# Kernel tuning notes

Hardware: AMD Instinct MI355X
Metric: run time of the kernel (lower is better)

The kernel has to match this reference:

```python
import jax, jax.numpy as jnp
import numpy as np

R, K, C, T = 4096, 16384, 512, 1000

def setup_inputs() -> dict:
    key = jax.random.key(0)
    k1, k2, k3, k4 = jax.random.split(key, 4)
    x = jax.random.normal(k1, (R, 1, C), dtype=jnp.float32)
    t = jax.random.randint(k2, (R,), 0, T)
    A = jax.random.normal(k3, (K, C), dtype=jnp.float32)
    # bar_alpha in (0,1): cumulative alpha-bar diffusion schedule
    bar_alpha = jax.random.uniform(k4, (T,), dtype=jnp.float32, minval=1e-4, maxval=1.0 - 1e-4)
    return {"x": x, "t": t, "A": A, "bar_alpha": bar_alpha}

def reference(x, t, A, bar_alpha):
    # x: [R,1,C], t: [R] int, A: [K,C] codebook, bar_alpha: [T]
    xs = x[:, 0, :]                       # [R,C]
    ba = bar_alpha[t]                     # [R]
    sa = jnp.sqrt(ba)                     # sqrt(bar_alpha[t_r])
    # ||sa_r*A_k - x_r||^2 = sa^2*||A_k||^2 - 2*sa*(x_r . A_k) + ||x_r||^2
    A_sq = jnp.sum(A * A, axis=1)         # [K]
    x_sq = jnp.sum(xs * xs, axis=1)       # [R]
    xA = jnp.einsum('rc,kc->rk', xs, A)   # [R,K]
    d2 = sa[:, None] ** 2 * A_sq[None, :] - 2.0 * sa[:, None] * xA + x_sq[:, None]
    logits = -d2 / (2.0 * (1.0 - ba))[:, None]   # [R,K]
    w = jax.nn.softmax(logits, axis=1)           # per-row softmax weights
    res = jnp.einsum('rk,kc->rc', w, A)          # [R,C]
    return res[:, None, :]                        # [R,1,C]
```

## Files before the change

kernel.cpp:

```cpp
#include <hip/hip_runtime.h>
#include <cstdint>
#include <cstddef>

#define R_DIM 4096
#define K_DIM 16384
#define C_DIM 512
#define SPLITS 4
#define BM 64
#define BK 128
#define KRANGE (K_DIM / SPLITS)
#define NTILES (KRANGE / BK)
#define GTILES (K_DIM / BK)

typedef unsigned short us8 __attribute__((ext_vector_type(8)));
typedef float f32x4 __attribute__((ext_vector_type(4)));
typedef __bf16 bfv8 __attribute__((ext_vector_type(8)));

#define MFMA16(a, b, c) __builtin_amdgcn_mfma_f32_16x16x32_bf16((a), (b), (c), 0, 0, 0)
#define BC(v) __builtin_bit_cast(bfv8, (v))

__device__ __forceinline__ unsigned short f2bf(float v) {
    union { float f; unsigned u; } x; x.f = v;
    unsigned r = x.u + 0x7fffu + ((x.u >> 16) & 1u);
    return (unsigned short)(r >> 16);
}
__device__ __forceinline__ float bf2f(unsigned short b) {
    union { unsigned u; float f; } x; x.u = ((unsigned)b) << 16;
    return x.f;
}

__device__ __forceinline__ void gload16(const char* g, char* l) {
    __builtin_amdgcn_global_load_lds(
        (const __attribute__((address_space(1))) void*)g,
        (__attribute__((address_space(3))) void*)l, 16, 0, 0);
}

#define PHASE_BAR(N) do {                                                   \
    asm volatile("s_waitcnt vmcnt(" #N ") lgkmcnt(0)" ::: "memory");        \
    __builtin_amdgcn_s_barrier();                                           \
    __builtin_amdgcn_sched_barrier(0);                                      \
} while (0)

#define OFF_IMGA ((size_t)0)
#define OFF_IMGC ((size_t)33554432)
#define OFF_XH   ((size_t)67108864)
#define OFF_XL   ((size_t)71303168)
#define OFF_ASQ  ((size_t)75497472)
#define OFF_ROWP ((size_t)75563008)
#define OFF_PO   ((size_t)75628544)
#define OFF_PM   ((size_t)109182976)
#define OFF_PL   ((size_t)109248512)
#define WS_NEED  ((size_t)109314048)

#define SM_BUF0 0
#define SM_BUF1 32768
#define SM_BUF2 65536
#define SM_U    98304
#define SM_U2   114688
#define SM_MX   131072
#define SM_SM   131584
#define SM_TOT  132096


__global__ void k_rows(const int* __restrict__ t, const float* __restrict__ bar_alpha,
                       float4* __restrict__ rowp) {
    int r = blockIdx.x * 256 + threadIdx.x;
    if (r >= R_DIM) return;
    float ba = bar_alpha[t[r]];
    float sa = sqrtf(ba);
    float inv = 1.0f / (1.0f - ba);
    rowp[r] = make_float4(sa, 0.5f * sa * sa, inv * 1.4426950408889634f, inv);
}

__global__ void k_splitx(const float* __restrict__ x, us8* __restrict__ xh, us8* __restrict__ xl) {
    int i = blockIdx.x * 256 + threadIdx.x;
    if (i >= R_DIM * C_DIM / 8) return;
    const float4* x4 = (const float4*)x + (size_t)i * 2;
    float v[8];
    float4 a = x4[0], b = x4[1];
    v[0]=a.x; v[1]=a.y; v[2]=a.z; v[3]=a.w; v[4]=b.x; v[5]=b.y; v[6]=b.z; v[7]=b.w;
    us8 h, l;
#pragma unroll
    for (int j = 0; j < 8; ++j) {
        unsigned short hb = f2bf(v[j]);
        h[j] = hb;
        l[j] = f2bf(v[j] - bf2f(hb));
    }
    xh[i] = h; xl[i] = l;
}

__global__ __launch_bounds__(256) void k_imgA(const float* __restrict__ A, char* __restrict__ img) {
    int gt = blockIdx.x >> 3, j = blockIdx.x & 7;
    char* base = img + (size_t)blockIdx.x * 32768;
    int t = threadIdx.x;
#pragma unroll
    for (int it = 0; it < 4; ++it) {
        int p = t + it * 256;
        int kl = p >> 3, cb = p & 7;
        const float* src = A + (size_t)(gt * 128 + kl) * C_DIM + j * 64 + cb * 8;
        us8 h, l;
#pragma unroll
        for (int q = 0; q < 8; ++q) {
            float v = src[q];
            unsigned short hb = f2bf(v);
            h[q] = hb; l[q] = f2bf(v - bf2f(hb));
        }
        int pos = kl * 128 + ((cb * 16) ^ ((kl & 7) << 4));
        *(us8*)(base + pos) = h;
        *(us8*)(base + 16384 + pos) = l;
    }
}

__global__ __launch_bounds__(256) void k_imgC(const float* __restrict__ A, char* __restrict__ img) {
    int gt = blockIdx.x >> 3, j = blockIdx.x & 7;
    char* base = img + (size_t)blockIdx.x * 32768;
    int t = threadIdx.x;
#pragma unroll
    for (int it = 0; it < 4; ++it) {
        int p = t + it * 256;
        int cl = p & 63, kb = p >> 6;
        us8 h, l;
#pragma unroll
        for (int q = 0; q < 8; ++q) {
            float v = A[(size_t)(gt * 128 + kb * 8 + q) * C_DIM + j * 64 + cl];
            unsigned short hb = f2bf(v);
            h[q] = hb; l[q] = f2bf(v - bf2f(hb));
        }
        int pos = cl * 256 + ((kb * 16) ^ ((cl & 7) << 4));
        *(us8*)(base + pos) = h;
        *(us8*)(base + 16384 + pos) = l;
    }
}

__global__ void k_asq(const float* __restrict__ A, float* __restrict__ Asq) {
    int wid = threadIdx.x >> 6, lane = threadIdx.x & 63;
    int k = blockIdx.x * 4 + wid;
    const float4* a4 = (const float4*)(A + (size_t)k * C_DIM);
    float s = 0.f;
#pragma unroll
    for (int j = 0; j < 2; ++j) {
        float4 v = a4[lane * 2 + j];
        s += v.x * v.x + v.y * v.y + v.z * v.z + v.w * v.w;
    }
#pragma unroll
    for (int off = 32; off; off >>= 1) s += __shfl_xor(s, off);
    if (lane == 0) Asq[k] = s;
}

__global__ __launch_bounds__(512, 2) void k_fused(
    const char* __restrict__ imgA, const char* __restrict__ imgC,
    const unsigned short* __restrict__ xh, const unsigned short* __restrict__ xl,
    const float* __restrict__ Asq, const float4* __restrict__ rowp,
    float* __restrict__ pO, float* __restrict__ pM, float* __restrict__ pL)
{
    extern __shared__ char smem[];
    const int tid = threadIdx.x;
    const int lane = tid & 63, wid = tid >> 6;
    const int wr = wid >> 1, wc = wid & 1;
    const int l15 = lane & 15, l4 = lane >> 4;
    const int rb = (blockIdx.x >> 2) * BM;
    const int split = blockIdx.x & (SPLITS - 1);

    float sa[4], hb[4], ce[4];
#pragma unroll
    for (int q = 0; q < 4; ++q) {
        float4 p = rowp[rb + wr * 16 + l4 * 4 + q];
        sa[q] = p.x; hb[q] = p.y; ce[q] = p.z;
    }
    float Mr[4], Lr[4];
#pragma unroll
    for (int q = 0; q < 4; ++q) { Mr[q] = -1e30f; Lr[q] = 0.f; }
    f32x4 of[8][2];
#pragma unroll
    for (int a = 0; a < 8; ++a)
#pragma unroll
        for (int b = 0; b < 2; ++b) of[a][b] = (f32x4){0.f, 0.f, 0.f, 0.f};

    const int xrow = (rb + wr * 16 + l15) * C_DIM;
    const int stg = tid * 16;

    {
        const char* s0 = imgA + (size_t)(split * NTILES) * 8 * 32768;
        const char* s1 = s0 + 32768;
#pragma unroll
        for (int i = 0; i < 4; ++i) gload16(s0 + stg + i * 8192, smem + SM_BUF0 + stg + i * 8192);
#pragma unroll
        for (int i = 0; i < 4; ++i) gload16(s1 + stg + i * 8192, smem + SM_BUF1 + stg + i * 8192);
    }
    __syncthreads();
    int cur = 0;

    for (int kt = 0; kt < NTILES; ++kt) {
        const int gt = split * NTILES + kt;
        const int gtn = (kt == NTILES - 1) ? split * NTILES : gt + 1;
        const int kbase = gt * BK;
        f32x4 sf[4];
#pragma unroll
        for (int f = 0; f < 4; ++f) sf[f] = (f32x4){0.f, 0.f, 0.f, 0.f};

        us8 xbh[2][2], xbl[2][2];
#pragma unroll
        for (int j = 0; j < 8; ++j) {
            if (j == 0) {
#pragma unroll
                for (int cs = 0; cs < 2; ++cs) {
                    int off = xrow + 0 * 64 + cs * 32 + l4 * 8;
                    xbh[0][cs] = *(const us8*)(xh + off);
                    xbl[0][cs] = *(const us8*)(xl + off);
                }
            }
            if (j < 7) {
#pragma unroll
                for (int cs = 0; cs < 2; ++cs) {
                    int off = xrow + (j + 1) * 64 + cs * 32 + l4 * 8;
                    xbh[(j + 1) & 1][cs] = *(const us8*)(xh + off);
                    xbl[(j + 1) & 1][cs] = *(const us8*)(xl + off);
                }
            }
            {
                char* d = smem + ((cur + 2) % 3) * 32768 + stg;
                if (j < 6) {
                    const char* s = imgA + ((size_t)gt * 8 + j + 2) * 32768;
#pragma unroll
                    for (int i = 0; i < 4; ++i) gload16(s + stg + i * 8192, d + i * 8192);
                } else if (j == 6) {
                    const char* s = imgC + ((size_t)gt * 8 + 0) * 32768;
#pragma unroll
                    for (int i = 0; i < 2; ++i) gload16(s + stg + i * 8192, d + i * 8192);
                } else {
                    const char* s = imgC + ((size_t)gt * 8 + 1) * 32768;
#pragma unroll
                    for (int i = 0; i < 2; ++i) gload16(s + stg + i * 8192, d + i * 8192);
                }
            }
            const char* B = smem + cur * 32768;
#pragma unroll
            for (int cs = 0; cs < 2; ++cs) {
#pragma unroll
                for (int f = 0; f < 4; ++f) {
                    int row = wc * 64 + f * 16 + l15;
                    int byte = row * 128 + ((cs * 64 + l4 * 16) ^ ((row & 7) << 4));
                    bfv8 qh = *(const bfv8*)(B + byte);
                    bfv8 ql = *(const bfv8*)(B + 16384 + byte);
                    sf[f] = MFMA16(BC(xbh[j & 1][cs]), qh, sf[f]);
                    sf[f] = MFMA16(BC(xbh[j & 1][cs]), ql, sf[f]);
                    sf[f] = MFMA16(BC(xbl[j & 1][cs]), qh, sf[f]);
                }
            }
            if (j == 0)      PHASE_BAR(8);
            else if (j < 6)  PHASE_BAR(6);
            else if (j == 6) PHASE_BAR(4);
            else             PHASE_BAR(2);
            cur = (cur + 1) % 3;
        }

        float g[4][4];
#pragma unroll
        for (int f = 0; f < 4; ++f) {
            float asq = Asq[kbase + wc * 64 + f * 16 + l15];
#pragma unroll
            for (int q = 0; q < 4; ++q) g[f][q] = sa[q] * sf[f][q] - hb[q] * asq;
        }
        float tmax[4];
#pragma unroll
        for (int q = 0; q < 4; ++q)
            tmax[q] = fmaxf(fmaxf(g[0][q], g[1][q]), fmaxf(g[2][q], g[3][q]));
#pragma unroll
        for (int off = 1; off < 16; off <<= 1)
#pragma unroll
            for (int q = 0; q < 4; ++q) tmax[q] = fmaxf(tmax[q], __shfl_xor(tmax[q], off));
        float* smax = (float*)(smem + SM_MX);
        if (l15 == 0) {
#pragma unroll
            for (int q = 0; q < 4; ++q) smax[wc * 64 + wr * 16 + l4 * 4 + q] = tmax[q];
        }
        __syncthreads();
        float Mn[4], al[4];
#pragma unroll
        for (int q = 0; q < 4; ++q) {
            float other = smax[(wc ^ 1) * 64 + wr * 16 + l4 * 4 + q];
            float tm = fmaxf(tmax[q], other);
            Mn[q] = fmaxf(Mr[q], tm);
            al[q] = exp2f((Mr[q] - Mn[q]) * ce[q]);
        }
        float u[4][4], tsum[4] = {0.f, 0.f, 0.f, 0.f};
#pragma unroll
        for (int f = 0; f < 4; ++f)
#pragma unroll
            for (int q = 0; q < 4; ++q) {
                u[f][q] = exp2f((g[f][q] - Mn[q]) * ce[q]);
                tsum[q] += u[f][q];
            }
#pragma unroll
        for (int off = 1; off < 16; off <<= 1)
#pragma unroll
            for (int q = 0; q < 4; ++q) tsum[q] += __shfl_xor(tsum[q], off);
        float* ssum = (float*)(smem + SM_SM);
        if (l15 == 0) {
#pragma unroll
            for (int q = 0; q < 4; ++q) ssum[wc * 64 + wr * 16 + l4 * 4 + q] = tsum[q];
        }
#pragma unroll
        for (int f = 0; f < 4; ++f)
#pragma unroll
            for (int q = 0; q < 4; ++q) {
                int m_loc = wr * 16 + l4 * 4 + q;
                int k_loc = wc * 64 + f * 16 + l15;
                int byte = (m_loc * 256 + k_loc * 2) ^ ((m_loc & 7) << 4);
                unsigned short uh = f2bf(u[f][q]);
                *(unsigned short*)(smem + SM_U + byte) = uh;
                *(unsigned short*)(smem + SM_U2 + byte) = f2bf(u[f][q] - bf2f(uh));
            }
        __syncthreads();
#pragma unroll
        for (int q = 0; q < 4; ++q) {
            float others = ssum[(wc ^ 1) * 64 + wr * 16 + l4 * 4 + q];
            Lr[q] = Lr[q] * al[q] + tsum[q] + others;
            Mr[q] = Mn[q];
        }
#pragma unroll
        for (int a = 0; a < 8; ++a)
#pragma unroll
            for (int b = 0; b < 2; ++b)
#pragma unroll
                for (int q = 0; q < 4; ++q) of[a][b][q] *= al[q];

        us8 uhf[4], ulf[4];
#pragma unroll
        for (int ks = 0; ks < 4; ++ks) {
            int m_loc = wr * 16 + l15;
            int byte = (m_loc * 256 + ks * 64 + l4 * 16) ^ ((m_loc & 7) << 4);
            uhf[ks] = *(const us8*)(smem + SM_U + byte);
            ulf[ks] = *(const us8*)(smem + SM_U2 + byte);
        }
#pragma unroll
        for (int j = 0; j < 8; ++j) {
            {
                char* d = smem + ((cur + 2) % 3) * 32768 + stg;
                if (j < 6) {
                    const char* s = imgC + ((size_t)gt * 8 + j + 2) * 32768;
#pragma unroll
                    for (int i = 0; i < 2; ++i) gload16(s + stg + i * 8192, d + i * 8192);
                } else {
                    const char* s = imgA + ((size_t)gtn * 8 + (j - 6)) * 32768;
#pragma unroll
                    for (int i = 0; i < 4; ++i) gload16(s + stg + i * 8192, d + i * 8192);
                }
            }
            const char* B = smem + cur * 32768;
#pragma unroll
            for (int f = 0; f < 2; ++f) {
                int cl = wc * 32 + f * 16 + l15;
#pragma unroll
                for (int ks = 0; ks < 4; ++ks) {
                    int byte = cl * 256 + ((ks * 64 + l4 * 16) ^ ((cl & 7) << 4));
                    bfv8 qh = *(const bfv8*)(B + byte);
                    of[j][f] = MFMA16(BC(uhf[ks]), qh, of[j][f]);
                    of[j][f] = MFMA16(BC(ulf[ks]), qh, of[j][f]);
                }
            }
            if (j < 6) PHASE_BAR(2);
            else       PHASE_BAR(4);
            cur = (cur + 1) % 3;
        }
    }

#pragma unroll
    for (int j = 0; j < 8; ++j)
#pragma unroll
        for (int f = 0; f < 2; ++f)
#pragma unroll
            for (int q = 0; q < 4; ++q) {
                int gm = rb + wr * 16 + l4 * 4 + q;
                int cg = j * 64 + wc * 32 + f * 16 + l15;
                pO[((size_t)gm * SPLITS + split) * C_DIM + cg] = of[j][f][q];
            }
    if (wc == 0 && l15 == 0) {
#pragma unroll
        for (int q = 0; q < 4; ++q) {
            int gm = rb + wr * 16 + l4 * 4 + q;
            pM[gm * SPLITS + split] = Mr[q];
            pL[gm * SPLITS + split] = Lr[q];
        }
    }
}

__global__ void k_combine(const float* __restrict__ pO, const float* __restrict__ pM,
                          const float* __restrict__ pL, const float4* __restrict__ rowp,
                          float* __restrict__ out) {
    int r = blockIdx.x;
    int tid = threadIdx.x;
    float ce = rowp[r].z;
    float Ms[SPLITS], Ls[SPLITS];
    float M = -1e30f;
#pragma unroll
    for (int s = 0; s < SPLITS; ++s) {
        Ms[s] = pM[r * SPLITS + s];
        Ls[s] = pL[r * SPLITS + s];
        M = fmaxf(M, Ms[s]);
    }
    float es[SPLITS], L = 0.f;
#pragma unroll
    for (int s = 0; s < SPLITS; ++s) { es[s] = exp2f((Ms[s] - M) * ce); L += Ls[s] * es[s]; }
    float invL = 1.0f / L;
    f32x4 acc = (f32x4){0.f, 0.f, 0.f, 0.f};
#pragma unroll
    for (int s = 0; s < SPLITS; ++s) {
        f32x4 v = *(const f32x4*)(pO + ((size_t)r * SPLITS + s) * C_DIM + tid * 4);
        acc += v * es[s];
    }
    acc *= invL;
    *(f32x4*)(out + (size_t)r * C_DIM + tid * 4) = acc;
}

extern "C" void kernel_launch(void* const* d_in, const int* in_sizes, int n_in,
                              void* d_out, int out_size, void* d_ws, size_t ws_size,
                              hipStream_t stream) {
    const float* x = (const float*)d_in[0];
    const int* t = (const int*)d_in[1];
    const float* A = (const float*)d_in[2];
    const float* bar_alpha = (const float*)d_in[3];
    float* out = (float*)d_out;
    char* ws = (char*)d_ws;
    if (ws_size < WS_NEED) return;

    char* imgA = ws + OFF_IMGA;
    char* imgC = ws + OFF_IMGC;
    unsigned short* Xh = (unsigned short*)(ws + OFF_XH);
    unsigned short* Xl = (unsigned short*)(ws + OFF_XL);
    float* Asq = (float*)(ws + OFF_ASQ);
    float4* rowp = (float4*)(ws + OFF_ROWP);
    float* pO = (float*)(ws + OFF_PO);
    float* pM = (float*)(ws + OFF_PM);
    float* pL = (float*)(ws + OFF_PL);

    (void)hipFuncSetAttribute((const void*)k_fused,
                              hipFuncAttributeMaxDynamicSharedMemorySize, SM_TOT);

    k_rows<<<R_DIM / 256, 256, 0, stream>>>(t, bar_alpha, rowp);
    k_splitx<<<(R_DIM * C_DIM / 8) / 256, 256, 0, stream>>>(x, (us8*)Xh, (us8*)Xl);
    k_imgA<<<GTILES * 8, 256, 0, stream>>>(A, imgA);
    k_imgC<<<GTILES * 8, 256, 0, stream>>>(A, imgC);
    k_asq<<<K_DIM / 4, 256, 0, stream>>>(A, Asq);
    k_fused<<<(R_DIM / BM) * SPLITS, 512, SM_TOT, stream>>>(imgA, imgC, Xh, Xl,
                                                            Asq, rowp, pO, pM, pL);
    k_combine<<<R_DIM, 128, 0, stream>>>(pO, pM, pL, rowp, out);
}
```

Before: 537.2 us.

## Switch fused softmax-attention kernel to 32x32x16 MFMA with 2x4 wave tiling

Rewrites the fused kernel to use 32x32x16 bf16 MFMA tiles instead of 16x16x32, remapping the eight waves from 4x2 to 2x4 (rows x keys). The per-wave fragment layout, the softmax max/sum reductions (now across four key-waves through shared memory), the P-matrix swizzled store, and the second GEMM's C-tile staging (two C chunks per phase, four phases) all change to match. The goal is fewer MFMA instructions and fewer LDS operand reads per FLOP. The cost is more registers per wave, wider 32-lane shuffle reductions, and a uniform phase barrier count.

```diff
diff --git a/kernel.cpp b/kernel.cpp
--- a/kernel.cpp
+++ b/kernel.cpp
@@ -14,9 +14,10 @@
 
 typedef unsigned short us8 __attribute__((ext_vector_type(8)));
 typedef float f32x4 __attribute__((ext_vector_type(4)));
+typedef float f32x16 __attribute__((ext_vector_type(16)));
 typedef __bf16 bfv8 __attribute__((ext_vector_type(8)));
 
-#define MFMA16(a, b, c) __builtin_amdgcn_mfma_f32_16x16x32_bf16((a), (b), (c), 0, 0, 0)
+#define MFMA32(a, b, c) __builtin_amdgcn_mfma_f32_32x32x16_bf16((a), (b), (c), 0, 0, 0)
 #define BC(v) __builtin_bit_cast(bfv8, (v))
 
 __device__ __forceinline__ unsigned short f2bf(float v) {
@@ -58,8 +59,9 @@
 #define SM_U    98304
 #define SM_U2   114688
 #define SM_MX   131072
-#define SM_SM   131584
-#define SM_TOT  132096
+#define SM_SM   132096
+#define SM_ROWL 133120
+#define SM_TOT  133632
 
 
 __global__ void k_rows(const int* __restrict__ t, const float* __restrict__ bar_alpha,
@@ -156,27 +158,30 @@
     extern __shared__ char smem[];
     const int tid = threadIdx.x;
     const int lane = tid & 63, wid = tid >> 6;
-    const int wr = wid >> 1, wc = wid & 1;
-    const int l15 = lane & 15, l4 = lane >> 4;
+    const int wm = wid >> 2, wk = wid & 3;
+    const int l31 = lane & 31, hl = lane >> 5;
     const int rb = (blockIdx.x >> 2) * BM;
     const int split = blockIdx.x & (SPLITS - 1);
 
-    float sa[4], hb[4], ce[4];
-#pragma unroll
-    for (int q = 0; q < 4; ++q) {
-        float4 p = rowp[rb + wr * 16 + l4 * 4 + q];
-        sa[q] = p.x; hb[q] = p.y; ce[q] = p.z;
-    }
-    float Mr[4], Lr[4];
-#pragma unroll
-    for (int q = 0; q < 4; ++q) { Mr[q] = -1e30f; Lr[q] = 0.f; }
-    f32x4 of[8][2];
-#pragma unroll
-    for (int a = 0; a < 8; ++a)
-#pragma unroll
-        for (int b = 0; b < 2; ++b) of[a][b] = (f32x4){0.f, 0.f, 0.f, 0.f};
-
-    const int xrow = (rb + wr * 16 + l15) * C_DIM;
+    float2* rowl = (float2*)(smem + SM_ROWL);
+    float* smax = (float*)(smem + SM_MX);
+    float* ssum = (float*)(smem + SM_SM);
+
+    if (tid < 64) {
+        float4 p = rowp[rb + tid];
+        rowl[tid] = make_float2(p.x, p.z);
+    }
+
+    float Mr[16], Lr[16];
+#pragma unroll
+    for (int r = 0; r < 16; ++r) { Mr[r] = -1e30f; Lr[r] = 0.f; }
+    f32x16 of[4];
+#pragma unroll
+    for (int p = 0; p < 4; ++p)
+#pragma unroll
+        for (int r = 0; r < 16; ++r) of[p][r] = 0.f;
+
+    const int xrowbase = (rb + wm * 32 + l31) * C_DIM;
     const int stg = tid * 16;
 
     {
@@ -194,193 +199,173 @@
         const int gt = split * NTILES + kt;
         const int gtn = (kt == NTILES - 1) ? split * NTILES : gt + 1;
         const int kbase = gt * BK;
-        f32x4 sf[4];
-#pragma unroll
-        for (int f = 0; f < 4; ++f) sf[f] = (f32x4){0.f, 0.f, 0.f, 0.f};
-
-        us8 xbh[2][2], xbl[2][2];
+
+        f32x16 sf;
+#pragma unroll
+        for (int r = 0; r < 16; ++r) sf[r] = 0.f;
+
 #pragma unroll
         for (int j = 0; j < 8; ++j) {
-            if (j == 0) {
-#pragma unroll
-                for (int cs = 0; cs < 2; ++cs) {
-                    int off = xrow + 0 * 64 + cs * 32 + l4 * 8;
-                    xbh[0][cs] = *(const us8*)(xh + off);
-                    xbl[0][cs] = *(const us8*)(xl + off);
-                }
-            }
-            if (j < 7) {
-#pragma unroll
-                for (int cs = 0; cs < 2; ++cs) {
-                    int off = xrow + (j + 1) * 64 + cs * 32 + l4 * 8;
-                    xbh[(j + 1) & 1][cs] = *(const us8*)(xh + off);
-                    xbl[(j + 1) & 1][cs] = *(const us8*)(xl + off);
-                }
-            }
+            us8 xh8[4], xl8[4];
+#pragma unroll
+            for (int s = 0; s < 4; ++s) {
+                int xoff = xrowbase + j * 64 + s * 16 + hl * 8;
+                xh8[s] = *(const us8*)(xh + xoff);
+                xl8[s] = *(const us8*)(xl + xoff);
+            }
+            __builtin_amdgcn_sched_barrier(0);
             {
-                char* d = smem + ((cur + 2) % 3) * 32768 + stg;
+                char* d = smem + ((cur + 2) % 3) * 32768;
                 if (j < 6) {
                     const char* s = imgA + ((size_t)gt * 8 + j + 2) * 32768;
 #pragma unroll
-                    for (int i = 0; i < 4; ++i) gload16(s + stg + i * 8192, d + i * 8192);
-                } else if (j == 6) {
-                    const char* s = imgC + ((size_t)gt * 8 + 0) * 32768;
-#pragma unroll
-                    for (int i = 0; i < 2; ++i) gload16(s + stg + i * 8192, d + i * 8192);
+                    for (int i = 0; i < 4; ++i) gload16(s + stg + i * 8192, d + stg + i * 8192);
                 } else {
-                    const char* s = imgC + ((size_t)gt * 8 + 1) * 32768;
-#pragma unroll
-                    for (int i = 0; i < 2; ++i) gload16(s + stg + i * 8192, d + i * 8192);
+                    int c0 = (j - 6) * 2;
+                    const char* s0 = imgC + ((size_t)gt * 8 + c0) * 32768;
+                    const char* s1 = imgC + ((size_t)gt * 8 + c0 + 1) * 32768;
+                    gload16(s0 + stg, d + stg);
+                    gload16(s0 + stg + 8192, d + stg + 8192);
+                    gload16(s1 + stg, d + 16384 + stg);
+                    gload16(s1 + stg + 8192, d + 16384 + stg + 8192);
                 }
             }
+            __builtin_amdgcn_sched_barrier(0);
             const char* B = smem + cur * 32768;
-#pragma unroll
-            for (int cs = 0; cs < 2; ++cs) {
-#pragma unroll
-                for (int f = 0; f < 4; ++f) {
-                    int row = wc * 64 + f * 16 + l15;
-                    int byte = row * 128 + ((cs * 64 + l4 * 16) ^ ((row & 7) << 4));
-                    bfv8 qh = *(const bfv8*)(B + byte);
-                    bfv8 ql = *(const bfv8*)(B + 16384 + byte);
-                    sf[f] = MFMA16(BC(xbh[j & 1][cs]), qh, sf[f]);
-                    sf[f] = MFMA16(BC(xbh[j & 1][cs]), ql, sf[f]);
-                    sf[f] = MFMA16(BC(xbl[j & 1][cs]), qh, sf[f]);
+            const int kl = wk * 32 + l31;
+#pragma unroll
+            for (int s = 0; s < 4; ++s) {
+                int cb = 2 * s + hl;
+                int byte = kl * 128 + ((cb ^ (kl & 7)) << 4);
+                bfv8 qh = *(const bfv8*)(B + byte);
+                bfv8 ql = *(const bfv8*)(B + 16384 + byte);
+                sf = MFMA32(BC(xh8[s]), qh, sf);
+                sf = MFMA32(BC(xh8[s]), ql, sf);
+                sf = MFMA32(BC(xl8[s]), qh, sf);
+            }
+            PHASE_BAR(4);
+            cur = (cur + 1) % 3;
+        }
+
+        {
+            const int k = wk * 32 + l31;
+            const float asq = Asq[kbase + k];
+            const int kb = k >> 3;
+            float g[16], mx[16];
+#pragma unroll
+            for (int r = 0; r < 16; ++r) {
+                int ml = wm * 32 + (r & 3) + 8 * (r >> 2) + 4 * hl;
+                float sa = rowl[ml].x;
+                g[r] = sa * (sf[r] - 0.5f * sa * asq);
+                mx[r] = g[r];
+            }
+#pragma unroll
+            for (int off = 1; off < 32; off <<= 1)
+#pragma unroll
+                for (int r = 0; r < 16; ++r) mx[r] = fmaxf(mx[r], __shfl_xor(mx[r], off));
+            if (l31 == 0) {
+#pragma unroll
+                for (int r = 0; r < 16; ++r)
+                    smax[wk * 64 + wm * 32 + (r & 3) + 8 * (r >> 2) + 4 * hl] = mx[r];
+            }
+            __syncthreads();
+            float Mn[16], al[16], ts[16];
+#pragma unroll
+            for (int r = 0; r < 16; ++r) {
+                int ml = wm * 32 + (r & 3) + 8 * (r >> 2) + 4 * hl;
+                float m4 = fmaxf(fmaxf(smax[ml], smax[64 + ml]),
+                                 fmaxf(smax[128 + ml], smax[192 + ml]));
+                Mn[r] = fmaxf(Mr[r], m4);
+                float ce = rowl[ml].y;
+                al[r] = exp2f((Mr[r] - Mn[r]) * ce);
+                float u = exp2f((g[r] - Mn[r]) * ce);
+                ts[r] = u;
+                unsigned short uh = f2bf(u);
+                unsigned short ul = f2bf(u - bf2f(uh));
+                int byte = ml * 256 + ((kb ^ (ml & 7)) << 4) + (k & 7) * 2;
+                *(unsigned short*)(smem + SM_U + byte) = uh;
+                *(unsigned short*)(smem + SM_U2 + byte) = ul;
+            }
+#pragma unroll
+            for (int off = 1; off < 32; off <<= 1)
+#pragma unroll
+                for (int r = 0; r < 16; ++r) ts[r] += __shfl_xor(ts[r], off);
+            if (l31 == 0) {
+#pragma unroll
+                for (int r = 0; r < 16; ++r)
+                    ssum[wk * 64 + wm * 32 + (r & 3) + 8 * (r >> 2) + 4 * hl] = ts[r];
+            }
+            __syncthreads();
+#pragma unroll
+            for (int r = 0; r < 16; ++r) {
+                int ml = wm * 32 + (r & 3) + 8 * (r >> 2) + 4 * hl;
+                float s4 = (ssum[ml] + ssum[64 + ml]) + (ssum[128 + ml] + ssum[192 + ml]);
+                Lr[r] = Lr[r] * al[r] + s4;
+                Mr[r] = Mn[r];
+            }
+#pragma unroll
+            for (int p = 0; p < 4; ++p)
+#pragma unroll
+                for (int r = 0; r < 16; ++r) of[p][r] *= al[r];
+        }
+        bfv8 uH[8], uL[8];
+        {
+            const int m2 = wm * 32 + l31;
+#pragma unroll
+            for (int ks = 0; ks < 8; ++ks) {
+                int kb2 = ks * 2 + hl;
+                int byte = m2 * 256 + ((kb2 ^ (m2 & 7)) << 4);
+                uH[ks] = *(const bfv8*)(smem + SM_U + byte);
+                uL[ks] = *(const bfv8*)(smem + SM_U2 + byte);
+            }
+        }
+
+#pragma unroll
+        for (int p = 0; p < 4; ++p) {
+            {
+                char* d = smem + ((cur + 2) % 3) * 32768;
+                if (p < 2) {
+                    const char* s0 = imgC + ((size_t)gt * 8 + (p + 2) * 2) * 32768;
+                    const char* s1 = imgC + ((size_t)gt * 8 + (p + 2) * 2 + 1) * 32768;
+                    gload16(s0 + stg, d + stg);
+                    gload16(s0 + stg + 8192, d + stg + 8192);
+                    gload16(s1 + stg, d + 16384 + stg);
+                    gload16(s1 + stg + 8192, d + 16384 + stg + 8192);
+                } else {
+                    const char* s = imgA + ((size_t)gtn * 8 + (p - 2)) * 32768;
+#pragma unroll
+                    for (int i = 0; i < 4; ++i) gload16(s + stg + i * 8192, d + stg + i * 8192);
                 }
             }
-            if (j == 0)      PHASE_BAR(8);
-            else if (j < 6)  PHASE_BAR(6);
-            else if (j == 6) PHASE_BAR(4);
-            else             PHASE_BAR(2);
+            const char* B = smem + cur * 32768 + (wk >> 1) * 16384;
+            const int cl = (wk & 1) * 32 + l31;
+#pragma unroll
+            for (int ks = 0; ks < 8; ++ks) {
+                int kb = ks * 2 + hl;
+                int byte = cl * 256 + ((kb ^ (cl & 7)) << 4);
+                bfv8 qh = *(const bfv8*)(B + byte);
+                of[p] = MFMA32(uH[ks], qh, of[p]);
+                of[p] = MFMA32(uL[ks], qh, of[p]);
+            }
+            PHASE_BAR(4);
             cur = (cur + 1) % 3;
         }
-
-        float g[4][4];
-#pragma unroll
-        for (int f = 0; f < 4; ++f) {
-            float asq = Asq[kbase + wc * 64 + f * 16 + l15];
-#pragma unroll
-            for (int q = 0; q < 4; ++q) g[f][q] = sa[q] * sf[f][q] - hb[q] * asq;
-        }
-        float tmax[4];
-#pragma unroll
-        for (int q = 0; q < 4; ++q)
-            tmax[q] = fmaxf(fmaxf(g[0][q], g[1][q]), fmaxf(g[2][q], g[3][q]));
-#pragma unroll
-        for (int off = 1; off < 16; off <<= 1)
-#pragma unroll
-            for (int q = 0; q < 4; ++q) tmax[q] = fmaxf(tmax[q], __shfl_xor(tmax[q], off));
-        float* smax = (float*)(smem + SM_MX);
-        if (l15 == 0) {
-#pragma unroll
-            for (int q = 0; q < 4; ++q) smax[wc * 64 + wr * 16 + l4 * 4 + q] = tmax[q];
-        }
-        __syncthreads();
-        float Mn[4], al[4];
-#pragma unroll
-        for (int q = 0; q < 4; ++q) {
-            float other = smax[(wc ^ 1) * 64 + wr * 16 + l4 * 4 + q];
-            float tm = fmaxf(tmax[q], other);
-            Mn[q] = fmaxf(Mr[q], tm);
-            al[q] = exp2f((Mr[q] - Mn[q]) * ce[q]);
-        }
-        float u[4][4], tsum[4] = {0.f, 0.f, 0.f, 0.f};
-#pragma unroll
-        for (int f = 0; f < 4; ++f)
-#pragma unroll
-            for (int q = 0; q < 4; ++q) {
-                u[f][q] = exp2f((g[f][q] - Mn[q]) * ce[q]);
-                tsum[q] += u[f][q];
-            }
-#pragma unroll
-        for (int off = 1; off < 16; off <<= 1)
-#pragma unroll
-            for (int q = 0; q < 4; ++q) tsum[q] += __shfl_xor(tsum[q], off);
-        float* ssum = (float*)(smem + SM_SM);
-        if (l15 == 0) {
-#pragma unroll
-            for (int q = 0; q < 4; ++q) ssum[wc * 64 + wr * 16 + l4 * 4 + q] = tsum[q];
-        }
-#pragma unroll
-        for (int f = 0; f < 4; ++f)
-#pragma unroll
-            for (int q = 0; q < 4; ++q) {
-                int m_loc = wr * 16 + l4 * 4 + q;
-                int k_loc = wc * 64 + f * 16 + l15;
-                int byte = (m_loc * 256 + k_loc * 2) ^ ((m_loc & 7) << 4);
-                unsigned short uh = f2bf(u[f][q]);
-                *(unsigned short*)(smem + SM_U + byte) = uh;
-                *(unsigned short*)(smem + SM_U2 + byte) = f2bf(u[f][q] - bf2f(uh));
-            }
-        __syncthreads();
-#pragma unroll
-        for (int q = 0; q < 4; ++q) {
-            float others = ssum[(wc ^ 1) * 64 + wr * 16 + l4 * 4 + q];
-            Lr[q] = Lr[q] * al[q] + tsum[q] + others;
-            Mr[q] = Mn[q];
-        }
-#pragma unroll
-        for (int a = 0; a < 8; ++a)
-#pragma unroll
-            for (int b = 0; b < 2; ++b)
-#pragma unroll
-                for (int q = 0; q < 4; ++q) of[a][b][q] *= al[q];
-
-        us8 uhf[4], ulf[4];
-#pragma unroll
-        for (int ks = 0; ks < 4; ++ks) {
-            int m_loc = wr * 16 + l15;
-            int byte = (m_loc * 256 + ks * 64 + l4 * 16) ^ ((m_loc & 7) << 4);
-            uhf[ks] = *(const us8*)(smem + SM_U + byte);
-            ulf[ks] = *(const us8*)(smem + SM_U2 + byte);
-        }
-#pragma unroll
-        for (int j = 0; j < 8; ++j) {
-            {
-                char* d = smem + ((cur + 2) % 3) * 32768 + stg;
-                if (j < 6) {
-                    const char* s = imgC + ((size_t)gt * 8 + j + 2) * 32768;
-#pragma unroll
-                    for (int i = 0; i < 2; ++i) gload16(s + stg + i * 8192, d + i * 8192);
-                } else {
-                    const char* s = imgA + ((size_t)gtn * 8 + (j - 6)) * 32768;
-#pragma unroll
-                    for (int i = 0; i < 4; ++i) gload16(s + stg + i * 8192, d + i * 8192);
-                }
-            }
-            const char* B = smem + cur * 32768;
-#pragma unroll
-            for (int f = 0; f < 2; ++f) {
-                int cl = wc * 32 + f * 16 + l15;
-#pragma unroll
-                for (int ks = 0; ks < 4; ++ks) {
-                    int byte = cl * 256 + ((ks * 64 + l4 * 16) ^ ((cl & 7) << 4));
-                    bfv8 qh = *(const bfv8*)(B + byte);
-                    of[j][f] = MFMA16(BC(uhf[ks]), qh, of[j][f]);
-                    of[j][f] = MFMA16(BC(ulf[ks]), qh, of[j][f]);
-                }
-            }
-            if (j < 6) PHASE_BAR(2);
-            else       PHASE_BAR(4);
-            cur = (cur + 1) % 3;
-        }
-    }
-
-#pragma unroll
-    for (int j = 0; j < 8; ++j)
-#pragma unroll
-        for (int f = 0; f < 2; ++f)
-#pragma unroll
-            for (int q = 0; q < 4; ++q) {
-                int gm = rb + wr * 16 + l4 * 4 + q;
-                int cg = j * 64 + wc * 32 + f * 16 + l15;
-                pO[((size_t)gm * SPLITS + split) * C_DIM + cg] = of[j][f][q];
-            }
-    if (wc == 0 && l15 == 0) {
-#pragma unroll
-        for (int q = 0; q < 4; ++q) {
-            int gm = rb + wr * 16 + l4 * 4 + q;
-            pM[gm * SPLITS + split] = Mr[q];
-            pL[gm * SPLITS + split] = Lr[q];
+    }
+
+#pragma unroll
+    for (int p = 0; p < 4; ++p)
+#pragma unroll
+        for (int r = 0; r < 16; ++r) {
+            int gm = rb + wm * 32 + (r & 3) + 8 * (r >> 2) + 4 * hl;
+            int cg = p * 128 + wk * 32 + l31;
+            pO[((size_t)gm * SPLITS + split) * C_DIM + cg] = of[p][r];
+        }
+    if (wk == 0 && l31 == 0) {
+#pragma unroll
+        for (int r = 0; r < 16; ++r) {
+            int gm = rb + wm * 32 + (r & 3) + 8 * (r >> 2) + 4 * hl;
+            pM[gm * SPLITS + split] = Mr[r];
+            pL[gm * SPLITS + split] = Lr[r];
         }
     }
 }
```

Measured after the change: 1.172 ms. 118% more time.

## Split QK phase across warps along C with 2 M-fragments and smem reduction

Applied to the files above, without the earlier changes.

Changes the score-GEMM warp layout so each warp covers 32 rows (two M fragments) and half of each C chunk, reusing every loaded A fragment for two MFMA groups and halving LDS B reads per MFMA. Partial scores from the two C-halves are reduced through a staging buffer in shared memory, and only half the warps do the softmax; rescale factors are shared via a new smem array. The x split kernel writes x in a permuted layout to match the new per-warp column slicing. This adds an extra barrier and smem round trip and leaves half the warps idle during softmax.

```diff
diff --git a/kernel.cpp b/kernel.cpp
--- a/kernel.cpp
+++ b/kernel.cpp
@@ -59,7 +59,8 @@
 #define SM_U2   114688
 #define SM_MX   131072
 #define SM_SM   131584
-#define SM_TOT  132096
+#define SM_AL   132096
+#define SM_TOT  132352
 
 
 __global__ void k_rows(const int* __restrict__ t, const float* __restrict__ bar_alpha,
@@ -75,18 +76,22 @@
 __global__ void k_splitx(const float* __restrict__ x, us8* __restrict__ xh, us8* __restrict__ xl) {
     int i = blockIdx.x * 256 + threadIdx.x;
     if (i >= R_DIM * C_DIM / 8) return;
+    int r = i >> 6;
+    int c = (i & 63) * 8;
+    int ct = (c >> 5) & 1, j = c >> 6, cp = c & 31;
+    int og = (r * 512 + ct * 256 + j * 32 + cp) >> 3;
     const float4* x4 = (const float4*)x + (size_t)i * 2;
     float v[8];
     float4 a = x4[0], b = x4[1];
     v[0]=a.x; v[1]=a.y; v[2]=a.z; v[3]=a.w; v[4]=b.x; v[5]=b.y; v[6]=b.z; v[7]=b.w;
     us8 h, l;
 #pragma unroll
-    for (int j = 0; j < 8; ++j) {
-        unsigned short hb = f2bf(v[j]);
-        h[j] = hb;
-        l[j] = f2bf(v[j] - bf2f(hb));
-    }
-    xh[i] = h; xl[i] = l;
+    for (int q = 0; q < 8; ++q) {
+        unsigned short hb = f2bf(v[q]);
+        h[q] = hb;
+        l[q] = f2bf(v[q] - bf2f(hb));
+    }
+    xh[og] = h; xl[og] = l;
 }
 
 __global__ __launch_bounds__(256) void k_imgA(const float* __restrict__ A, char* __restrict__ img) {
@@ -156,27 +161,32 @@
     extern __shared__ char smem[];
     const int tid = threadIdx.x;
     const int lane = tid & 63, wid = tid >> 6;
-    const int wr = wid >> 1, wc = wid & 1;
+    const int wr2 = wid >> 2, wc = (wid >> 1) & 1, ct = wid & 1;
+    const int wrC = wid >> 1, wcC = wid & 1;
     const int l15 = lane & 15, l4 = lane >> 4;
     const int rb = (blockIdx.x >> 2) * BM;
     const int split = blockIdx.x & (SPLITS - 1);
 
-    float sa[4], hb[4], ce[4];
-#pragma unroll
-    for (int q = 0; q < 4; ++q) {
-        float4 p = rowp[rb + wr * 16 + l4 * 4 + q];
-        sa[q] = p.x; hb[q] = p.y; ce[q] = p.z;
-    }
-    float Mr[4], Lr[4];
-#pragma unroll
-    for (int q = 0; q < 4; ++q) { Mr[q] = -1e30f; Lr[q] = 0.f; }
+    float sa[2][4], hb[2][4], ce[2][4];
+#pragma unroll
+    for (int mf = 0; mf < 2; ++mf)
+#pragma unroll
+        for (int q = 0; q < 4; ++q) {
+            float4 p = rowp[rb + wr2 * 32 + mf * 16 + l4 * 4 + q];
+            sa[mf][q] = p.x; hb[mf][q] = p.y; ce[mf][q] = p.z;
+        }
+    float Mr[2][4], Lr[2][4];
+#pragma unroll
+    for (int mf = 0; mf < 2; ++mf)
+#pragma unroll
+        for (int q = 0; q < 4; ++q) { Mr[mf][q] = -1e30f; Lr[mf][q] = 0.f; }
     f32x4 of[8][2];
 #pragma unroll
     for (int a = 0; a < 8; ++a)
 #pragma unroll
         for (int b = 0; b < 2; ++b) of[a][b] = (f32x4){0.f, 0.f, 0.f, 0.f};
 
-    const int xrow = (rb + wr * 16 + l15) * C_DIM;
+    const int xb0 = (rb + wr2 * 32 + l15) * 512 + ct * 256 + l4 * 8;
     const int stg = tid * 16;
 
     {
@@ -194,29 +204,21 @@
         const int gt = split * NTILES + kt;
         const int gtn = (kt == NTILES - 1) ? split * NTILES : gt + 1;
         const int kbase = gt * BK;
-        f32x4 sf[4];
-#pragma unroll
-        for (int f = 0; f < 4; ++f) sf[f] = (f32x4){0.f, 0.f, 0.f, 0.f};
+        f32x4 sf[2][4];
+#pragma unroll
+        for (int mf = 0; mf < 2; ++mf)
+#pragma unroll
+            for (int f = 0; f < 4; ++f) sf[mf][f] = (f32x4){0.f, 0.f, 0.f, 0.f};
 
         us8 xbh[2][2], xbl[2][2];
 #pragma unroll
+        for (int mf = 0; mf < 2; ++mf) {
+            int off = xb0 + mf * 8192;
+            xbh[0][mf] = *(const us8*)(xh + off);
+            xbl[0][mf] = *(const us8*)(xl + off);
+        }
+#pragma unroll
         for (int j = 0; j < 8; ++j) {
-            if (j == 0) {
-#pragma unroll
-                for (int cs = 0; cs < 2; ++cs) {
-                    int off = xrow + 0 * 64 + cs * 32 + l4 * 8;
-                    xbh[0][cs] = *(const us8*)(xh + off);
-                    xbl[0][cs] = *(const us8*)(xl + off);
-                }
-            }
-            if (j < 7) {
-#pragma unroll
-                for (int cs = 0; cs < 2; ++cs) {
-                    int off = xrow + (j + 1) * 64 + cs * 32 + l4 * 8;
-                    xbh[(j + 1) & 1][cs] = *(const us8*)(xh + off);
-                    xbl[(j + 1) & 1][cs] = *(const us8*)(xl + off);
-                }
-            }
             {
                 char* d = smem + ((cur + 2) % 3) * 32768 + stg;
                 if (j < 6) {
@@ -233,18 +235,26 @@
                     for (int i = 0; i < 2; ++i) gload16(s + stg + i * 8192, d + i * 8192);
                 }
             }
+            if (j < 7) {
+#pragma unroll
+                for (int mf = 0; mf < 2; ++mf) {
+                    int off = xb0 + mf * 8192 + (j + 1) * 32;
+                    xbh[(j + 1) & 1][mf] = *(const us8*)(xh + off);
+                    xbl[(j + 1) & 1][mf] = *(const us8*)(xl + off);
+                }
+            }
             const char* B = smem + cur * 32768;
 #pragma unroll
-            for (int cs = 0; cs < 2; ++cs) {
-#pragma unroll
-                for (int f = 0; f < 4; ++f) {
-                    int row = wc * 64 + f * 16 + l15;
-                    int byte = row * 128 + ((cs * 64 + l4 * 16) ^ ((row & 7) << 4));
-                    bfv8 qh = *(const bfv8*)(B + byte);
-                    bfv8 ql = *(const bfv8*)(B + 16384 + byte);
-                    sf[f] = MFMA16(BC(xbh[j & 1][cs]), qh, sf[f]);
-                    sf[f] = MFMA16(BC(xbh[j & 1][cs]), ql, sf[f]);
-                    sf[f] = MFMA16(BC(xbl[j & 1][cs]), qh, sf[f]);
+            for (int f = 0; f < 4; ++f) {
+                int row = wc * 64 + f * 16 + l15;
+                int byte = row * 128 + ((ct * 64 + l4 * 16) ^ ((row & 7) << 4));
+                bfv8 qh = *(const bfv8*)(B + byte);
+                bfv8 ql = *(const bfv8*)(B + 16384 + byte);
+#pragma unroll
+                for (int mf = 0; mf < 2; ++mf) {
+                    sf[mf][f] = MFMA16(BC(xbh[j & 1][mf]), qh, sf[mf][f]);
+                    sf[mf][f] = MFMA16(BC(xbh[j & 1][mf]), ql, sf[mf][f]);
+                    sf[mf][f] = MFMA16(BC(xbl[j & 1][mf]), qh, sf[mf][f]);
                 }
             }
             if (j == 0)      PHASE_BAR(8);
@@ -254,85 +264,130 @@
             cur = (cur + 1) % 3;
         }
 
-        float g[4][4];
-#pragma unroll
-        for (int f = 0; f < 4; ++f) {
-            float asq = Asq[kbase + wc * 64 + f * 16 + l15];
-#pragma unroll
-            for (int q = 0; q < 4; ++q) g[f][q] = sa[q] * sf[f][q] - hb[q] * asq;
-        }
-        float tmax[4];
-#pragma unroll
-        for (int q = 0; q < 4; ++q)
-            tmax[q] = fmaxf(fmaxf(g[0][q], g[1][q]), fmaxf(g[2][q], g[3][q]));
-#pragma unroll
-        for (int off = 1; off < 16; off <<= 1)
-#pragma unroll
-            for (int q = 0; q < 4; ++q) tmax[q] = fmaxf(tmax[q], __shfl_xor(tmax[q], off));
+        float* mrg = (float*)(smem + ((cur + 2) % 3) * 32768);
+        const int mslot = ((wr2 * 2 + wc) * 64 + lane) * 4;
+        if (ct == 1) {
+#pragma unroll
+            for (int mf = 0; mf < 2; ++mf)
+#pragma unroll
+                for (int f = 0; f < 4; ++f)
+                    *(f32x4*)(mrg + (mf * 4 + f) * 1024 + mslot) = sf[mf][f];
+        }
+        __syncthreads();
+
         float* smax = (float*)(smem + SM_MX);
-        if (l15 == 0) {
-#pragma unroll
-            for (int q = 0; q < 4; ++q) smax[wc * 64 + wr * 16 + l4 * 4 + q] = tmax[q];
+        float* ssum = (float*)(smem + SM_SM);
+        float* alL = (float*)(smem + SM_AL);
+        float g[2][4][4], Mn[2][4], al[2][4], ts[2][4];
+        if (ct == 0) {
+            float asq[4];
+#pragma unroll
+            for (int f = 0; f < 4; ++f) asq[f] = Asq[kbase + wc * 64 + f * 16 + l15];
+            float tmax[2][4];
+#pragma unroll
+            for (int mf = 0; mf < 2; ++mf)
+#pragma unroll
+                for (int f = 0; f < 4; ++f) {
+                    sf[mf][f] += *(const f32x4*)(mrg + (mf * 4 + f) * 1024 + mslot);
+#pragma unroll
+                    for (int q = 0; q < 4; ++q)
+                        g[mf][f][q] = sa[mf][q] * sf[mf][f][q] - hb[mf][q] * asq[f];
+                }
+#pragma unroll
+            for (int mf = 0; mf < 2; ++mf)
+#pragma unroll
+                for (int q = 0; q < 4; ++q)
+                    tmax[mf][q] = fmaxf(fmaxf(g[mf][0][q], g[mf][1][q]),
+                                        fmaxf(g[mf][2][q], g[mf][3][q]));
+#pragma unroll
+            for (int off = 1; off < 16; off <<= 1)
+#pragma unroll
+                for (int mf = 0; mf < 2; ++mf)
+#pragma unroll
+                    for (int q = 0; q < 4; ++q)
+                        tmax[mf][q] = fmaxf(tmax[mf][q], __shfl_xor(tmax[mf][q], off));
+            if (l15 == 0) {
+#pragma unroll
+                for (int mf = 0; mf < 2; ++mf)
+#pragma unroll
+                    for (int q = 0; q < 4; ++q)
+                        smax[wc * 64 + wr2 * 32 + mf * 16 + l4 * 4 + q] = tmax[mf][q];
+            }
         }
         __syncthreads();
-        float Mn[4], al[4];
-#pragma unroll
-        for (int q = 0; q < 4; ++q) {
-            float other = smax[(wc ^ 1) * 64 + wr * 16 + l4 * 4 + q];
-            float tm = fmaxf(tmax[q], other);
-            Mn[q] = fmaxf(Mr[q], tm);
-            al[q] = exp2f((Mr[q] - Mn[q]) * ce[q]);
-        }
-        float u[4][4], tsum[4] = {0.f, 0.f, 0.f, 0.f};
-#pragma unroll
-        for (int f = 0; f < 4; ++f)
-#pragma unroll
-            for (int q = 0; q < 4; ++q) {
-                u[f][q] = exp2f((g[f][q] - Mn[q]) * ce[q]);
-                tsum[q] += u[f][q];
-            }
-#pragma unroll
-        for (int off = 1; off < 16; off <<= 1)
-#pragma unroll
-            for (int q = 0; q < 4; ++q) tsum[q] += __shfl_xor(tsum[q], off);
-        float* ssum = (float*)(smem + SM_SM);
-        if (l15 == 0) {
-#pragma unroll
-            for (int q = 0; q < 4; ++q) ssum[wc * 64 + wr * 16 + l4 * 4 + q] = tsum[q];
-        }
-#pragma unroll
-        for (int f = 0; f < 4; ++f)
-#pragma unroll
-            for (int q = 0; q < 4; ++q) {
-                int m_loc = wr * 16 + l4 * 4 + q;
-                int k_loc = wc * 64 + f * 16 + l15;
-                int byte = (m_loc * 256 + k_loc * 2) ^ ((m_loc & 7) << 4);
-                unsigned short uh = f2bf(u[f][q]);
-                *(unsigned short*)(smem + SM_U + byte) = uh;
-                *(unsigned short*)(smem + SM_U2 + byte) = f2bf(u[f][q] - bf2f(uh));
-            }
+        if (ct == 0) {
+#pragma unroll
+            for (int mf = 0; mf < 2; ++mf)
+#pragma unroll
+                for (int q = 0; q < 4; ++q) {
+                    int row = wr2 * 32 + mf * 16 + l4 * 4 + q;
+                    float tm = fmaxf(smax[row], smax[64 + row]);
+                    Mn[mf][q] = fmaxf(Mr[mf][q], tm);
+                    al[mf][q] = exp2f((Mr[mf][q] - Mn[mf][q]) * ce[mf][q]);
+                    ts[mf][q] = 0.f;
+                }
+#pragma unroll
+            for (int mf = 0; mf < 2; ++mf)
+#pragma unroll
+                for (int f = 0; f < 4; ++f)
+#pragma unroll
+                    for (int q = 0; q < 4; ++q) {
+                        float u = exp2f((g[mf][f][q] - Mn[mf][q]) * ce[mf][q]);
+                        ts[mf][q] += u;
+                        int m_loc = wr2 * 32 + mf * 16 + l4 * 4 + q;
+                        int k_loc = wc * 64 + f * 16 + l15;
+                        int byte = (m_loc * 256 + k_loc * 2) ^ ((m_loc & 7) << 4);
+                        unsigned short uh = f2bf(u);
+                        *(unsigned short*)(smem + SM_U + byte) = uh;
+                        *(unsigned short*)(smem + SM_U2 + byte) = f2bf(u - bf2f(uh));
+                    }
+#pragma unroll
+            for (int off = 1; off < 16; off <<= 1)
+#pragma unroll
+                for (int mf = 0; mf < 2; ++mf)
+#pragma unroll
+                    for (int q = 0; q < 4; ++q) ts[mf][q] += __shfl_xor(ts[mf][q], off);
+            if (l15 == 0) {
+#pragma unroll
+                for (int mf = 0; mf < 2; ++mf)
+#pragma unroll
+                    for (int q = 0; q < 4; ++q) {
+                        int row = wr2 * 32 + mf * 16 + l4 * 4 + q;
+                        ssum[wc * 64 + row] = ts[mf][q];
+                        if (wc == 0) alL[row] = al[mf][q];
+                    }
+            }
+        }
         __syncthreads();
-#pragma unroll
-        for (int q = 0; q < 4; ++q) {
-            float others = ssum[(wc ^ 1) * 64 + wr * 16 + l4 * 4 + q];
-            Lr[q] = Lr[q] * al[q] + tsum[q] + others;
-            Mr[q] = Mn[q];
-        }
+        if (ct == 0) {
+#pragma unroll
+            for (int mf = 0; mf < 2; ++mf)
+#pragma unroll
+                for (int q = 0; q < 4; ++q) {
+                    int row = wr2 * 32 + mf * 16 + l4 * 4 + q;
+                    float others = ssum[(wc ^ 1) * 64 + row];
+                    Lr[mf][q] = Lr[mf][q] * al[mf][q] + ts[mf][q] + others;
+                    Mr[mf][q] = Mn[mf][q];
+                }
+        }
+        float alr[4];
+#pragma unroll
+        for (int q = 0; q < 4; ++q) alr[q] = alL[wrC * 16 + l4 * 4 + q];
 #pragma unroll
         for (int a = 0; a < 8; ++a)
 #pragma unroll
             for (int b = 0; b < 2; ++b)
 #pragma unroll
-                for (int q = 0; q < 4; ++q) of[a][b][q] *= al[q];
-
+                for (int q = 0; q < 4; ++q) of[a][b][q] *= alr[q];
         us8 uhf[4], ulf[4];
 #pragma unroll
         for (int ks = 0; ks < 4; ++ks) {
-            int m_loc = wr * 16 + l15;
+            int m_loc = wrC * 16 + l15;
             int byte = (m_loc * 256 + ks * 64 + l4 * 16) ^ ((m_loc & 7) << 4);
             uhf[ks] = *(const us8*)(smem + SM_U + byte);
             ulf[ks] = *(const us8*)(smem + SM_U2 + byte);
         }
+
 #pragma unroll
         for (int j = 0; j < 8; ++j) {
             {
@@ -349,14 +404,14 @@
             }
             const char* B = smem + cur * 32768;
 #pragma unroll
-            for (int f = 0; f < 2; ++f) {
-                int cl = wc * 32 + f * 16 + l15;
+            for (int f2 = 0; f2 < 2; ++f2) {
+                int cl = wcC * 32 + f2 * 16 + l15;
 #pragma unroll
                 for (int ks = 0; ks < 4; ++ks) {
                     int byte = cl * 256 + ((ks * 64 + l4 * 16) ^ ((cl & 7) << 4));
                     bfv8 qh = *(const bfv8*)(B + byte);
-                    of[j][f] = MFMA16(BC(uhf[ks]), qh, of[j][f]);
-                    of[j][f] = MFMA16(BC(ulf[ks]), qh, of[j][f]);
+                    of[j][f2] = MFMA16(BC(uhf[ks]), qh, of[j][f2]);
+                    of[j][f2] = MFMA16(BC(ulf[ks]), qh, of[j][f2]);
                 }
             }
             if (j < 6) PHASE_BAR(2);
@@ -368,20 +423,22 @@
 #pragma unroll
     for (int j = 0; j < 8; ++j)
 #pragma unroll
-        for (int f = 0; f < 2; ++f)
+        for (int f2 = 0; f2 < 2; ++f2)
 #pragma unroll
             for (int q = 0; q < 4; ++q) {
-                int gm = rb + wr * 16 + l4 * 4 + q;
-                int cg = j * 64 + wc * 32 + f * 16 + l15;
-                pO[((size_t)gm * SPLITS + split) * C_DIM + cg] = of[j][f][q];
-            }
-    if (wc == 0 && l15 == 0) {
-#pragma unroll
-        for (int q = 0; q < 4; ++q) {
-            int gm = rb + wr * 16 + l4 * 4 + q;
-            pM[gm * SPLITS + split] = Mr[q];
-            pL[gm * SPLITS + split] = Lr[q];
-        }
+                int gm = rb + wrC * 16 + l4 * 4 + q;
+                int cg = j * 64 + wcC * 32 + f2 * 16 + l15;
+                pO[((size_t)gm * SPLITS + split) * C_DIM + cg] = of[j][f2][q];
+            }
+    if (ct == 0 && wc == 0 && l15 == 0) {
+#pragma unroll
+        for (int mf = 0; mf < 2; ++mf)
+#pragma unroll
+            for (int q = 0; q < 4; ++q) {
+                int gm = rb + wr2 * 32 + mf * 16 + l4 * 4 + q;
+                pM[gm * SPLITS + split] = Mr[mf][q];
+                pL[gm * SPLITS + split] = Lr[mf][q];
+            }
     }
 }
 
```

New measurement: 899.1 us. 1.67x slower.
